# Performance work log

Measured on AMD Instinct MI355X. Metric: run time of the kernel, lower is better.

## Reference

```python
import jax, jax.numpy as jnp
from jax import lax
import numpy as np

B, Hd, Wd, Cd, D, HID = 64, 16, 16, 32, 64, 256


def setup_inputs() -> dict:
    key = jax.random.key(0)
    k0, k1, k2, k3, k4 = jax.random.split(key, 5)
    std = 1.0 / np.sqrt(HID)
    x = jax.random.normal(k0, (B, Hd, Wd, Cd, D), dtype=jnp.float32)
    # Linear weights stored as (in, out); torch Linear computes x @ W.T + b
    W_in = jax.random.uniform(k1, (D, HID), jnp.float32, -std, std)
    b_in = jax.random.uniform(k2, (HID,), jnp.float32, -std, std)
    W_h = jax.random.uniform(k3, (3 * HID, HID), jnp.float32, -std, std)
    b_h = jax.random.uniform(k4, (HID,), jnp.float32, -std, std)
    return {"x": x, "W_in": W_in, "b_in": b_in, "W_h": W_h, "b_h": b_h}


def reference(x, W_in, b_in, W_h, b_h):
    b, h, w, c, d = x.shape
    H = W_in.shape[1]
    # Precompute input projection for all positions (same math, hoisted out of loops)
    xp = jnp.einsum('bhwcd,dk->bhwck', x, W_in) + b_in  # (b,h,w,c,H)
    xp = jnp.transpose(xp, (1, 2, 3, 0, 4))             # (h,w,c,b,H)
    # Split hidden_layer weight by which previous-state block it multiplies:
    # cat(h_prev1, h_prev2, h_prev3) @ W_h = h1@W1 + h2@W2 + h3@W3
    W1, W2, W3 = W_h[:H], W_h[H:2 * H], W_h[2 * H:]

    def scan_k(h_k, inp):
        xp_k, h_up, h_left = inp  # each (b,H)
        hid = jnp.tanh(xp_k + h_up @ W1 + h_left @ W2 + h_k @ W3 + b_h)
        return hid, hid

    def scan_j(h_left_col, inp):
        xp_j, h_up_col = inp  # (c,b,H)
        zero = jnp.zeros((b, H), xp_j.dtype)
        _, h_col = lax.scan(scan_k, zero, (xp_j, h_up_col, h_left_col))
        return h_col, h_col  # (c,b,H)

    def scan_i(h_up_plane, xp_i):
        zero_col = jnp.zeros((c, b, H), xp_i.dtype)
        _, plane = lax.scan(scan_j, zero_col, (xp_i, h_up_plane))
        return plane, plane  # (w,c,b,H)

    zero_plane = jnp.zeros((w, c, b, H), x.dtype)
    _, hidden = lax.scan(scan_i, zero_plane, xp)  # (h,w,c,b,H)
    return jnp.transpose(hidden, (3, 0, 1, 2, 4))  # (b,h,w,c,H)
```

## Files before the change

kernel.cpp:

```cpp
#include <hip/hip_runtime.h>


typedef _Float16 f16x8 __attribute__((ext_vector_type(8)));
typedef float f32x4 __attribute__((ext_vector_type(4)));

#define OUT_BSTRIDE 2097152
#define X_BSTRIDE   524288
#define SLOT_BYTES  32768
#define FLAGS_OFF   1048576
#define RING3_OFF   2097152
#define RING3_BYTES ((size_t)8192 * SLOT_BYTES)
#define SMEM_BYTES  106496
#define FB_PITCH    260

__device__ __forceinline__ void bar_raw() {
  asm volatile("" ::: "memory");
  __builtin_amdgcn_s_barrier();
  asm volatile("" ::: "memory");
}
__device__ __forceinline__ void bar_lgkm() {
  asm volatile("s_waitcnt lgkmcnt(0)" ::: "memory");
  __builtin_amdgcn_sched_barrier(0);
  bar_raw();
}
__device__ __forceinline__ void bar_vm() {
  asm volatile("s_waitcnt vmcnt(0)" ::: "memory");
  __builtin_amdgcn_sched_barrier(0);
  bar_raw();
}

__device__ __forceinline__ void store_wt16(void* p, f16x8 v) {
  asm volatile("global_store_dwordx4 %0, %1, off sc0 sc1" :: "v"(p), "v"(v) : "memory");
}

__device__ __forceinline__ void wait_flag(const unsigned int* f) {
  while (__hip_atomic_load(f, __ATOMIC_RELAXED, __HIP_MEMORY_SCOPE_SYSTEM) == 0u)
    __builtin_amdgcn_s_sleep(2);
  asm volatile("" ::: "memory");
}

__device__ __forceinline__ f16x8 conv8f16(const f32x4& a, const f32x4& b) {
  f16x8 r;
  r[0] = (_Float16)a[0]; r[1] = (_Float16)a[1];
  r[2] = (_Float16)a[2]; r[3] = (_Float16)a[3];
  r[4] = (_Float16)b[0]; r[5] = (_Float16)b[1];
  r[6] = (_Float16)b[2]; r[7] = (_Float16)b[3];
  return r;
}

#define GL_AS1(p) ((const __attribute__((address_space(1))) unsigned int*)(p))
#define LDS_AS3(p) ((__attribute__((address_space(3))) unsigned int*)(p))

__device__ __forceinline__ void gll_copy4(const unsigned char* slot, unsigned char* buf,
                                          int w, int lane) {
#pragma unroll
  for (int it = 0; it < 4; ++it) {
    const unsigned char* g = slot + it * 8192 + w * 1024 + lane * 16;
    unsigned char* l = buf + it * 8192 + w * 1024;
    __builtin_amdgcn_global_load_lds(GL_AS1(g), LDS_AS3(l), 16, 0, 0);
  }
}

template<int KS, int PITCH>
__device__ __forceinline__ void mm1(f32x4 (&acc)[4][2], const unsigned char* smem,
                                    const _Float16* __restrict__ wt,
                                    int ncol0, int l15, int l4, int swz) {
#pragma unroll
  for (int kk = 0; kk < KS / 32; ++kk) {
    const int k0 = kk * 32 + l4 * 8;
    f16x8 ah[4], bh[2];
#pragma unroll
    for (int mi = 0; mi < 4; ++mi) {
      int byte = (mi * 16 + l15) * PITCH + ((k0 * 2) ^ swz);
      ah[mi] = *(const f16x8*)(smem + byte);
    }
#pragma unroll
    for (int ni = 0; ni < 2; ++ni) {
      int n = ncol0 + ni * 16 + l15;
      bh[ni] = *(const f16x8*)(wt + n * KS + k0);
    }
#pragma unroll
    for (int mi = 0; mi < 4; ++mi)
#pragma unroll
      for (int ni = 0; ni < 2; ++ni)
        acc[mi][ni] = __builtin_amdgcn_mfma_f32_16x16x32_f16(ah[mi], bh[ni], acc[mi][ni], 0, 0, 0);
  }
}

template<int KS, int PITCH>
__device__ __forceinline__ void mm1r(f32x4 (&acc)[4][2], const unsigned char* smem,
                                     const f16x8 (&bh)[KS / 32][2],
                                     int l15, int l4, int swz) {
#pragma unroll
  for (int kk = 0; kk < KS / 32; ++kk) {
    const int k0 = kk * 32 + l4 * 8;
    f16x8 ah[4];
#pragma unroll
    for (int mi = 0; mi < 4; ++mi) {
      int byte = (mi * 16 + l15) * PITCH + ((k0 * 2) ^ swz);
      ah[mi] = *(const f16x8*)(smem + byte);
    }
#pragma unroll
    for (int mi = 0; mi < 4; ++mi)
#pragma unroll
      for (int ni = 0; ni < 2; ++ni)
        acc[mi][ni] = __builtin_amdgcn_mfma_f32_16x16x32_f16(ah[mi], bh[kk][ni], acc[mi][ni], 0, 0, 0);
  }
}

template<int BPR, int ITERS, int PITCH>
__device__ __forceinline__ void stage_f16(const float* __restrict__ src, int rstride,
                                          unsigned char* buf, int t) {
#pragma unroll
  for (int it = 0; it < ITERS; ++it) {
    int c = t + it * 512;
    int row = c / BPR, bk = c % BPR;
    const float* p = src + row * rstride + bk * 8;
    f32x4 v0 = *(const f32x4*)p;
    f32x4 v1 = *(const f32x4*)(p + 4);
    f16x8 h8 = conv8f16(v0, v1);
    int byte = row * PITCH + ((bk * 16) ^ ((row & 7) << 4));
    *(f16x8*)(buf + byte) = h8;
  }
}

__global__ void mdrnn_prep(const float* __restrict__ W_in, const float* __restrict__ b_in,
                           const float* __restrict__ W_h, const float* __restrict__ b_h,
                           unsigned char* __restrict__ ws) {
  int t = blockIdx.x * 256 + threadIdx.x;
  float* bias = (float*)ws;
  _Float16* win = (_Float16*)(ws + 1024);
  _Float16* wh0 = win + 16384;

  if (t < 256) bias[t] = b_in[t] + b_h[t];
  if (t < 8192)
    __hip_atomic_store((unsigned int*)(ws + FLAGS_OFF) + t, 0u,
                       __ATOMIC_RELAXED, __HIP_MEMORY_SCOPE_SYSTEM);
  if (t < 16384) {
    int n = t >> 6, k = t & 63;
    win[t] = (_Float16)W_in[k * 256 + n];
  }
  if (t < 196608) {
    int m = t >> 16;
    int r = t & 65535;
    int n = r >> 8, k = r & 255;
    (wh0 + m * 65536)[r] = (_Float16)W_h[(m * 256 + k) * 256 + n];
  }
}

__global__ __launch_bounds__(512, 2)
void mdrnn_persist(const float* __restrict__ x, const unsigned char* __restrict__ ws,
                   unsigned char* __restrict__ ring, unsigned int* __restrict__ flags,
                   float* __restrict__ out) {
  const int bx = blockIdx.x;
  const int i = bx >> 4, j = bx & 15;

  __shared__ __align__(16) unsigned char smem[SMEM_BYTES];
  unsigned char* P = smem;
  unsigned char* R = smem + 32768;
  unsigned char* L = smem + 65536;
  unsigned char* X = smem + 98304;
  float* fbuf = (float*)(smem + 32768);

  const int t = threadIdx.x;
  const int lane = t & 63;
  const int w = t >> 6;
  const int l15 = lane & 15, l4 = lane >> 4;
  const int swz = (lane & 7) << 4;
  const int ncol0 = w * 32;

  const float* bias = (const float*)ws;
  const _Float16* win = (const _Float16*)(ws + 1024);
  const _Float16* w1 = win + 16384;
  const _Float16* w2 = w1 + 65536;
  const _Float16* w3 = w2 + 65536;

  const int cell2 = bx;
  const unsigned int* upF   = flags + (size_t)(cell2 - 16) * 32;
  const unsigned int* leftF = flags + (size_t)(cell2 - 1) * 32;
  unsigned int* myF = flags + (size_t)cell2 * 32;
  const bool has_cons = (i < 15) || (j < 15);

  f16x8 wbI[2][2], wb3[8][2];
#pragma unroll
  for (int kk = 0; kk < 2; ++kk)
#pragma unroll
    for (int ni = 0; ni < 2; ++ni) {
      int n = ncol0 + ni * 16 + l15;
      wbI[kk][ni] = *(const f16x8*)(win + n * 64 + kk * 32 + l4 * 8);
    }
#pragma unroll
  for (int kk = 0; kk < 8; ++kk)
#pragma unroll
    for (int ni = 0; ni < 2; ++ni) {
      int n = ncol0 + ni * 16 + l15;
      wb3[kk][ni] = *(const f16x8*)(w3 + n * 256 + kk * 32 + l4 * 8);
    }

  const int xrow = t >> 3, xck = t & 7;
  const float* xbase = x + (size_t)xrow * X_BSTRIDE + (size_t)cell2 * 32 * 64 + xck * 8;
  f32x4 xr0 = __builtin_nontemporal_load((const f32x4*)xbase);
  f32x4 xr1 = __builtin_nontemporal_load((const f32x4*)(xbase + 4));

  f32x4 vo0[4], vo1[4];

  for (int k = 0; k < 32; ++k) {
    const int cell3 = cell2 * 32 + k;

    {
      f16x8 h8 = conv8f16(xr0, xr1);
      int byte = xrow * 128 + ((xck * 16) ^ ((xrow & 7) << 4));
      *(f16x8*)(X + byte) = h8;
    }
    bar_lgkm();

    f32x4 acc[4][2];
#pragma unroll
    for (int mi = 0; mi < 4; ++mi)
#pragma unroll
      for (int ni = 0; ni < 2; ++ni)
        acc[mi][ni] = f32x4{0.f, 0.f, 0.f, 0.f};

    if (k > 0) {
      float* oc = out + (size_t)(cell3 - 1) * 256;
#pragma unroll
      for (int it = 0; it < 4; ++it) {
        int c = t + it * 512;
        int row = c >> 5, ck = c & 31;
        float* op = oc + (size_t)row * OUT_BSTRIDE + ck * 8;
        __builtin_nontemporal_store(vo0[it], (f32x4*)op);
        __builtin_nontemporal_store(vo1[it], (f32x4*)(op + 4));
      }
    }

    if (i > 0 && t == 0)  wait_flag(upF + k);
    if (j > 0 && t == 64) wait_flag(leftF + k);
    bar_raw();
    __builtin_amdgcn_sched_barrier(0);
    if (i > 0) gll_copy4(ring + (size_t)((cell2 - 16) * 32 + k) * SLOT_BYTES, R, w, lane);
    if (j > 0) gll_copy4(ring + (size_t)((cell2 - 1) * 32 + k) * SLOT_BYTES, L, w, lane);
    {
      int kn = (k < 31) ? k + 1 : 31;
      xr0 = __builtin_nontemporal_load((const f32x4*)(xbase + kn * 64));
      xr1 = __builtin_nontemporal_load((const f32x4*)(xbase + kn * 64 + 4));
    }
    __builtin_amdgcn_sched_barrier(0);

    mm1r<64, 128>(acc, X, wbI, l15, l4, swz);
    if (k > 0) mm1r<256, 512>(acc, P, wb3, l15, l4, swz);

    if (i > 0) {
      if (j > 0) { asm volatile("s_waitcnt vmcnt(6)" ::: "memory"); }
      else       { asm volatile("s_waitcnt vmcnt(2)" ::: "memory"); }
      __builtin_amdgcn_sched_barrier(0);
      bar_raw();
      mm1<256, 512>(acc, R, w1, ncol0, l15, l4, swz);
    }
    if (j > 0) {
      asm volatile("s_waitcnt vmcnt(2)" ::: "memory");
      __builtin_amdgcn_sched_barrier(0);
      bar_raw();
      mm1<256, 512>(acc, L, w2, ncol0, l15, l4, swz);
    }

    bar_raw();
#pragma unroll
    for (int mi = 0; mi < 4; ++mi)
#pragma unroll
      for (int ni = 0; ni < 2; ++ni) {
        int col = ncol0 + ni * 16 + l15;
        float bv = bias[col];
#pragma unroll
        for (int r = 0; r < 4; ++r) {
          int row = mi * 16 + l4 * 4 + r;
          float v = acc[mi][ni][r] + bv;
          float e = __expf(2.f * v);
          fbuf[row * FB_PITCH + col] = 1.f - 2.f / (e + 1.f);
        }
      }
    bar_lgkm();

    unsigned char* slotW = ring + (size_t)cell3 * SLOT_BYTES;
#pragma unroll
    for (int it = 0; it < 4; ++it) {
      int c = t + it * 512;
      int row = c >> 5, ck = c & 31;
      const float* p = fbuf + row * FB_PITCH + ck * 8;
      f32x4 v0 = *(const f32x4*)p;
      f32x4 v1 = *(const f32x4*)(p + 4);
      vo0[it] = v0;
      vo1[it] = v1;
      f16x8 h8 = conv8f16(v0, v1);
      int byte = row * 512 + ((ck * 16) ^ ((row & 7) << 4));
      *(f16x8*)(P + byte) = h8;
      if (has_cons) store_wt16(slotW + byte, h8);
    }

    bar_vm();
    if (has_cons && t == 0)
      __hip_atomic_store(myF + k, 1u, __ATOMIC_RELAXED, __HIP_MEMORY_SCOPE_SYSTEM);
  }

  {
    float* oc = out + (size_t)(cell2 * 32 + 31) * 256;
#pragma unroll
    for (int it = 0; it < 4; ++it) {
      int c = t + it * 512;
      int row = c >> 5, ck = c & 31;
      float* op = oc + (size_t)row * OUT_BSTRIDE + ck * 8;
      __builtin_nontemporal_store(vo0[it], (f32x4*)op);
      __builtin_nontemporal_store(vo1[it], (f32x4*)(op + 4));
    }
  }
}

__global__ __launch_bounds__(512)
void mdrnn_cell2(int s, const float* __restrict__ x, const unsigned char* __restrict__ ws,
                 float* __restrict__ out) {
  const int bx = blockIdx.x;
  const int i = bx >> 4, j = bx & 15;
  const int kc = s - i - j;
  if (kc < 0 || kc >= 32) return;

  __shared__ __align__(16) unsigned char smem[SMEM_BYTES];
  const int t = threadIdx.x;
  const int lane = t & 63;
  const int w = t >> 6;
  const int l15 = lane & 15, l4 = lane >> 4;
  const int swz = (lane & 7) << 4;
  const int ncol0 = w * 32;
  unsigned char* ABUF = smem;
  unsigned char* XBUF = smem + 32768;
  float* fbuf = (float*)smem;

  const float* bias = (const float*)ws;
  const _Float16* win = (const _Float16*)(ws + 1024);
  const _Float16* w1 = win + 16384;
  const _Float16* w2 = w1 + 65536;
  const _Float16* w3 = w2 + 65536;

  const int cell3 = (i * 16 + j) * 32 + kc;

  f32x4 acc[4][2];
#pragma unroll
  for (int mi = 0; mi < 4; ++mi)
#pragma unroll
    for (int ni = 0; ni < 2; ++ni)
      acc[mi][ni] = f32x4{0.f, 0.f, 0.f, 0.f};

  stage_f16<8, 1, 128>(x + (size_t)cell3 * 64, X_BSTRIDE, XBUF, t);
  bar_lgkm();
  mm1<64, 128>(acc, XBUF, win, ncol0, l15, l4, swz);

  if (j > 0) {
    bar_raw();
    stage_f16<32, 4, 512>(out + (size_t)(cell3 - 32) * 256, OUT_BSTRIDE, ABUF, t);
    bar_lgkm();
    mm1<256, 512>(acc, ABUF, w2, ncol0, l15, l4, swz);
  }
  if (i > 0) {
    bar_raw();
    stage_f16<32, 4, 512>(out + (size_t)(cell3 - 512) * 256, OUT_BSTRIDE, ABUF, t);
    bar_lgkm();
    mm1<256, 512>(acc, ABUF, w1, ncol0, l15, l4, swz);
  }
  if (kc > 0) {
    bar_raw();
    stage_f16<32, 4, 512>(out + (size_t)(cell3 - 1) * 256, OUT_BSTRIDE, ABUF, t);
    bar_lgkm();
    mm1<256, 512>(acc, ABUF, w3, ncol0, l15, l4, swz);
  }

  bar_raw();
#pragma unroll
  for (int mi = 0; mi < 4; ++mi)
#pragma unroll
    for (int ni = 0; ni < 2; ++ni) {
      int col = ncol0 + ni * 16 + l15;
      float bv = bias[col];
#pragma unroll
      for (int r = 0; r < 4; ++r) {
        int row = mi * 16 + l4 * 4 + r;
        float v = acc[mi][ni][r] + bv;
        float e = __expf(2.f * v);
        fbuf[row * FB_PITCH + col] = 1.f - 2.f / (e + 1.f);
      }
    }
  bar_lgkm();
#pragma unroll
  for (int it = 0; it < 4; ++it) {
    int c = t + it * 512;
    int row = c >> 5, ck = c & 31;
    const float* p = fbuf + row * FB_PITCH + ck * 8;
    f32x4 v0 = *(const f32x4*)p;
    f32x4 v1 = *(const f32x4*)(p + 4);
    float* op = out + (size_t)row * OUT_BSTRIDE + (size_t)cell3 * 256 + ck * 8;
    *(f32x4*)op = v0;
    *(f32x4*)(op + 4) = v1;
  }
}

extern "C" void kernel_launch(void* const* d_in, const int* in_sizes, int n_in,
                              void* d_out, int out_size, void* d_ws, size_t ws_size,
                              hipStream_t stream) {
  const float* x    = (const float*)d_in[0];
  const float* W_in = (const float*)d_in[1];
  const float* b_in = (const float*)d_in[2];
  const float* W_h  = (const float*)d_in[3];
  const float* b_h  = (const float*)d_in[4];
  float* out = (float*)d_out;
  unsigned char* ws = (unsigned char*)d_ws;

  mdrnn_prep<<<768, 256, 0, stream>>>(W_in, b_in, W_h, b_h, ws);

  if (ws_size >= (size_t)RING3_OFF + RING3_BYTES) {
    mdrnn_persist<<<256, 512, 0, stream>>>(x, ws, ws + RING3_OFF,
                                           (unsigned int*)(ws + FLAGS_OFF), out);
  } else {
    for (int s = 0; s <= 61; ++s)
      mdrnn_cell2<<<256, 512, 0, stream>>>(s, x, ws, out);
  }
}
```

Before: 916.9 us.

## Retile persistent MDRNN warps to 2x4 grid and write tanh directly as f16

Changes the per-wave output tile from 64 rows by 32 columns to 32 rows by 64 columns (2x4 wave grid), which halves A-fragment LDS reads per MFMA and doubles the register-resident W3 slice. The tanh epilogue now writes f16 directly into the P buffer instead of going through an fp32 staging buffer, and the output is re-expanded from f16 for the global store. It also drops the register-cached input weights in favour of reading them from memory, moves the input projection after the recurrent products, and pins waves per EU. Risks are higher register pressure, output values now rounded to f16 precision, and scattered 2-byte LDS stores in the epilogue.

```diff
diff --git a/kernel.cpp b/kernel.cpp
--- a/kernel.cpp
+++ b/kernel.cpp
@@ -62,6 +62,52 @@
 }
 
 template<int KS, int PITCH>
+__device__ __forceinline__ void mmB(f32x4 (&acc)[2][4], const unsigned char* smem,
+                                    const _Float16* __restrict__ wt,
+                                    int arow0, int ncol0, int l15, int l4, int swz) {
+#pragma unroll
+  for (int kk = 0; kk < KS / 32; ++kk) {
+    const int k0 = kk * 32 + l4 * 8;
+    f16x8 ah[2], bh[4];
+#pragma unroll
+    for (int mi = 0; mi < 2; ++mi) {
+      int byte = (arow0 + mi * 16 + l15) * PITCH + ((k0 * 2) ^ swz);
+      ah[mi] = *(const f16x8*)(smem + byte);
+    }
+#pragma unroll
+    for (int ni = 0; ni < 4; ++ni) {
+      int n = ncol0 + ni * 16 + l15;
+      bh[ni] = *(const f16x8*)(wt + n * KS + k0);
+    }
+#pragma unroll
+    for (int mi = 0; mi < 2; ++mi)
+#pragma unroll
+      for (int ni = 0; ni < 4; ++ni)
+        acc[mi][ni] = __builtin_amdgcn_mfma_f32_16x16x32_f16(ah[mi], bh[ni], acc[mi][ni], 0, 0, 0);
+  }
+}
+
+__device__ __forceinline__ void mmR(f32x4 (&acc)[2][4], const unsigned char* smem,
+                                    const f16x8 (&wb)[8][4],
+                                    int arow0, int l15, int l4, int swz) {
+#pragma unroll
+  for (int kk = 0; kk < 8; ++kk) {
+    const int k0 = kk * 32 + l4 * 8;
+    f16x8 ah[2];
+#pragma unroll
+    for (int mi = 0; mi < 2; ++mi) {
+      int byte = (arow0 + mi * 16 + l15) * 512 + ((k0 * 2) ^ swz);
+      ah[mi] = *(const f16x8*)(smem + byte);
+    }
+#pragma unroll
+    for (int mi = 0; mi < 2; ++mi)
+#pragma unroll
+      for (int ni = 0; ni < 4; ++ni)
+        acc[mi][ni] = __builtin_amdgcn_mfma_f32_16x16x32_f16(ah[mi], wb[kk][ni], acc[mi][ni], 0, 0, 0);
+  }
+}
+
+template<int KS, int PITCH>
 __device__ __forceinline__ void mm1(f32x4 (&acc)[4][2], const unsigned char* smem,
                                     const _Float16* __restrict__ wt,
                                     int ncol0, int l15, int l4, int swz) {
@@ -84,27 +130,6 @@
 #pragma unroll
       for (int ni = 0; ni < 2; ++ni)
         acc[mi][ni] = __builtin_amdgcn_mfma_f32_16x16x32_f16(ah[mi], bh[ni], acc[mi][ni], 0, 0, 0);
-  }
-}
-
-template<int KS, int PITCH>
-__device__ __forceinline__ void mm1r(f32x4 (&acc)[4][2], const unsigned char* smem,
-                                     const f16x8 (&bh)[KS / 32][2],
-                                     int l15, int l4, int swz) {
-#pragma unroll
-  for (int kk = 0; kk < KS / 32; ++kk) {
-    const int k0 = kk * 32 + l4 * 8;
-    f16x8 ah[4];
-#pragma unroll
-    for (int mi = 0; mi < 4; ++mi) {
-      int byte = (mi * 16 + l15) * PITCH + ((k0 * 2) ^ swz);
-      ah[mi] = *(const f16x8*)(smem + byte);
-    }
-#pragma unroll
-    for (int mi = 0; mi < 4; ++mi)
-#pragma unroll
-      for (int ni = 0; ni < 2; ++ni)
-        acc[mi][ni] = __builtin_amdgcn_mfma_f32_16x16x32_f16(ah[mi], bh[kk][ni], acc[mi][ni], 0, 0, 0);
   }
 }
 
@@ -148,7 +173,7 @@
   }
 }
 
-__global__ __launch_bounds__(512, 2)
+__global__ __launch_bounds__(512, 2) __attribute__((amdgpu_waves_per_eu(2, 2)))
 void mdrnn_persist(const float* __restrict__ x, const unsigned char* __restrict__ ws,
                    unsigned char* __restrict__ ring, unsigned int* __restrict__ flags,
                    float* __restrict__ out) {
@@ -160,14 +185,15 @@
   unsigned char* R = smem + 32768;
   unsigned char* L = smem + 65536;
   unsigned char* X = smem + 98304;
-  float* fbuf = (float*)(smem + 32768);
 
   const int t = threadIdx.x;
   const int lane = t & 63;
   const int w = t >> 6;
   const int l15 = lane & 15, l4 = lane >> 4;
   const int swz = (lane & 7) << 4;
-  const int ncol0 = w * 32;
+  const int wr = w >> 2, wc = w & 3;
+  const int arow0 = wr * 32;
+  const int ncol0 = wc * 64;
 
   const float* bias = (const float*)ws;
   const _Float16* win = (const _Float16*)(ws + 1024);
@@ -181,28 +207,24 @@
   unsigned int* myF = flags + (size_t)cell2 * 32;
   const bool has_cons = (i < 15) || (j < 15);
 
-  f16x8 wbI[2][2], wb3[8][2];
-#pragma unroll
-  for (int kk = 0; kk < 2; ++kk)
-#pragma unroll
-    for (int ni = 0; ni < 2; ++ni) {
-      int n = ncol0 + ni * 16 + l15;
-      wbI[kk][ni] = *(const f16x8*)(win + n * 64 + kk * 32 + l4 * 8);
-    }
+  f16x8 wb3[8][4];
 #pragma unroll
   for (int kk = 0; kk < 8; ++kk)
 #pragma unroll
-    for (int ni = 0; ni < 2; ++ni) {
+    for (int ni = 0; ni < 4; ++ni) {
       int n = ncol0 + ni * 16 + l15;
       wb3[kk][ni] = *(const f16x8*)(w3 + n * 256 + kk * 32 + l4 * 8);
     }
+  float bias4[4];
+#pragma unroll
+  for (int ni = 0; ni < 4; ++ni) bias4[ni] = bias[ncol0 + ni * 16 + l15];
 
   const int xrow = t >> 3, xck = t & 7;
   const float* xbase = x + (size_t)xrow * X_BSTRIDE + (size_t)cell2 * 32 * 64 + xck * 8;
   f32x4 xr0 = __builtin_nontemporal_load((const f32x4*)xbase);
   f32x4 xr1 = __builtin_nontemporal_load((const f32x4*)(xbase + 4));
 
-  f32x4 vo0[4], vo1[4];
+  f16x8 vo16[4];
 
   for (int k = 0; k < 32; ++k) {
     const int cell3 = cell2 * 32 + k;
@@ -214,11 +236,11 @@
     }
     bar_lgkm();
 
-    f32x4 acc[4][2];
-#pragma unroll
-    for (int mi = 0; mi < 4; ++mi)
-#pragma unroll
-      for (int ni = 0; ni < 2; ++ni)
+    f32x4 acc[2][4];
+#pragma unroll
+    for (int mi = 0; mi < 2; ++mi)
+#pragma unroll
+      for (int ni = 0; ni < 4; ++ni)
         acc[mi][ni] = f32x4{0.f, 0.f, 0.f, 0.f};
 
     if (k > 0) {
@@ -227,9 +249,12 @@
       for (int it = 0; it < 4; ++it) {
         int c = t + it * 512;
         int row = c >> 5, ck = c & 31;
+        f16x8 h = vo16[it];
+        f32x4 a{(float)h[0], (float)h[1], (float)h[2], (float)h[3]};
+        f32x4 b{(float)h[4], (float)h[5], (float)h[6], (float)h[7]};
         float* op = oc + (size_t)row * OUT_BSTRIDE + ck * 8;
-        __builtin_nontemporal_store(vo0[it], (f32x4*)op);
-        __builtin_nontemporal_store(vo1[it], (f32x4*)(op + 4));
+        __builtin_nontemporal_store(a, (f32x4*)op);
+        __builtin_nontemporal_store(b, (f32x4*)(op + 4));
       }
     }
 
@@ -246,36 +271,38 @@
     }
     __builtin_amdgcn_sched_barrier(0);
 
-    mm1r<64, 128>(acc, X, wbI, l15, l4, swz);
-    if (k > 0) mm1r<256, 512>(acc, P, wb3, l15, l4, swz);
+    if (k > 0) mmR(acc, P, wb3, arow0, l15, l4, swz);
 
     if (i > 0) {
       if (j > 0) { asm volatile("s_waitcnt vmcnt(6)" ::: "memory"); }
       else       { asm volatile("s_waitcnt vmcnt(2)" ::: "memory"); }
       __builtin_amdgcn_sched_barrier(0);
       bar_raw();
-      mm1<256, 512>(acc, R, w1, ncol0, l15, l4, swz);
+      mmB<256, 512>(acc, R, w1, arow0, ncol0, l15, l4, swz);
     }
     if (j > 0) {
       asm volatile("s_waitcnt vmcnt(2)" ::: "memory");
       __builtin_amdgcn_sched_barrier(0);
       bar_raw();
-      mm1<256, 512>(acc, L, w2, ncol0, l15, l4, swz);
-    }
+      mmB<256, 512>(acc, L, w2, arow0, ncol0, l15, l4, swz);
+    }
+
+    mmB<64, 128>(acc, X, win, arow0, ncol0, l15, l4, swz);
 
     bar_raw();
 #pragma unroll
-    for (int mi = 0; mi < 4; ++mi)
-#pragma unroll
-      for (int ni = 0; ni < 2; ++ni) {
+    for (int mi = 0; mi < 2; ++mi)
+#pragma unroll
+      for (int ni = 0; ni < 4; ++ni) {
+        float bv = bias4[ni];
         int col = ncol0 + ni * 16 + l15;
-        float bv = bias[col];
 #pragma unroll
         for (int r = 0; r < 4; ++r) {
-          int row = mi * 16 + l4 * 4 + r;
+          int row = arow0 + mi * 16 + l4 * 4 + r;
           float v = acc[mi][ni][r] + bv;
           float e = __expf(2.f * v);
-          fbuf[row * FB_PITCH + col] = 1.f - 2.f / (e + 1.f);
+          float th = 1.f - 2.f / (e + 1.f);
+          *(_Float16*)(P + row * 512 + ((col * 2) ^ ((row & 7) << 4))) = (_Float16)th;
         }
       }
     bar_lgkm();
@@ -285,14 +312,9 @@
     for (int it = 0; it < 4; ++it) {
       int c = t + it * 512;
       int row = c >> 5, ck = c & 31;
-      const float* p = fbuf + row * FB_PITCH + ck * 8;
-      f32x4 v0 = *(const f32x4*)p;
-      f32x4 v1 = *(const f32x4*)(p + 4);
-      vo0[it] = v0;
-      vo1[it] = v1;
-      f16x8 h8 = conv8f16(v0, v1);
       int byte = row * 512 + ((ck * 16) ^ ((row & 7) << 4));
-      *(f16x8*)(P + byte) = h8;
+      f16x8 h8 = *(const f16x8*)(P + byte);
+      vo16[it] = h8;
       if (has_cons) store_wt16(slotW + byte, h8);
     }
 
@@ -307,9 +329,12 @@
     for (int it = 0; it < 4; ++it) {
       int c = t + it * 512;
       int row = c >> 5, ck = c & 31;
+      f16x8 h = vo16[it];
+      f32x4 a{(float)h[0], (float)h[1], (float)h[2], (float)h[3]};
+      f32x4 b{(float)h[4], (float)h[5], (float)h[6], (float)h[7]};
       float* op = oc + (size_t)row * OUT_BSTRIDE + ck * 8;
-      __builtin_nontemporal_store(vo0[it], (f32x4*)op);
-      __builtin_nontemporal_store(vo1[it], (f32x4*)(op + 4));
+      __builtin_nontemporal_store(a, (f32x4*)op);
+      __builtin_nontemporal_store(b, (f32x4*)(op + 4));
     }
   }
 }
```

Result: slower. 2.110 ms (+130.1%).
